# Kernel tuning notes

Measured on AMD Instinct MI355X. Metric: run time of the kernel, lower is better.

The kernel has to match this reference:

```python
import jax, jax.numpy as jnp
import numpy as np

B, NB, L, K, C, H = 4, 256, 64, 65, 512, 8
HD = C // H
SCALE = HD ** -0.5


def setup_inputs() -> dict:
    key = jax.random.key(0)
    k = jax.random.split(key, 6)
    x = jax.random.normal(k[0], (B, NB * L, C), dtype=jnp.float32)
    mask = jax.random.bernoulli(k[1], 0.3, (NB, L, K))
    d = jnp.arange(L)
    mask = mask.at[:, d, d].set(True)      # self edges always on
    mask = mask.at[:, :, L].set(True)      # block-node column always on
    edge_feats = jax.random.normal(k[2], (NB, L, K, 4), dtype=jnp.float32)
    qkv_w = jax.random.normal(k[3], (C, 3 * C), dtype=jnp.float32) * (C ** -0.5)
    qkv_b = jnp.zeros((3 * C,), dtype=jnp.float32)
    proj_w = jax.random.normal(k[4], (C, C), dtype=jnp.float32) * (C ** -0.5)
    proj_b = jnp.zeros((C,), dtype=jnp.float32)
    return {"x": x, "attn_mask": mask, "edge_feats": edge_feats,
            "qkv_w": qkv_w, "qkv_b": qkv_b, "proj_w": proj_w, "proj_b": proj_b}


def reference(x, attn_mask, edge_feats, qkv_w, qkv_b, proj_w, proj_b):
    # x: (B, N, C) with N = NB*L (no padding needed); pool = 1, layout LxL+1
    x_blk = x.reshape(B, NB, L, C)                       # query tokens per leaf block
    block_node = x_blk.mean(axis=2, keepdims=True)       # (B, NB, 1, C)
    kv = jnp.concatenate([x_blk, block_node], axis=2)    # (B, NB, K, C), K = L+1

    qkv_q = x_blk @ qkv_w + qkv_b
    qkv_kv = kv @ qkv_w + qkv_b
    q = qkv_q[..., :C].reshape(B, NB, L, H, HD)
    k = qkv_kv[..., C:2 * C].reshape(B, NB, K, H, HD)
    v = qkv_kv[..., 2 * C:].reshape(B, NB, K, H, HD)

    scores = jnp.einsum('bnqhd,bnkhd->bnqkh', q, k) * SCALE  # (B,NB,L,K,H)

    # physics bias: edge_feats[..., :4] broadcast over batch; special/diagonal overrides
    bp = jnp.broadcast_to(edge_feats[None, ..., :4], (B, NB, L, K, 4))
    bp = bp.at[:, :, :, L, :].set(0.0)
    bp = bp.at[:, :, :, L, 3].set(1.0)                    # block-node key column
    d = jnp.arange(L)
    bp = bp.at[:, :, d, d, :].set(0.0)
    bp = bp.at[:, :, d, d, 3].set(1.0)                    # self edge
    scores = scores + bp[..., 3:4]                        # channel 3 additive bias (all heads)

    mask = attn_mask[None, :, :, :, None]                 # (1,NB,L,K,1)
    scores = jnp.where(mask, scores, jnp.float32(-1e9))
    attn = jax.nn.softmax(scores, axis=3)

    out = jnp.einsum('bnqkh,bnkhd->bnqhd', attn, v).reshape(B, NB * L, C)
    return out @ proj_w + proj_b
```

## Files before the change

### kernel.cpp

```cpp
#include <hip/hip_runtime.h>
#include <hip/hip_bf16.h>
#include <math.h>

typedef unsigned short u16;
typedef __attribute__((ext_vector_type(8))) short s16x8;
typedef __attribute__((ext_vector_type(4))) float f32x4;

#define NB_ 256
#define L_  64
#define KK_ 65
#define C_  512
#define H_  8
#define NEDGE (256*64*65)
#define MTOT  65536
#define MEXT  66560

__device__ __forceinline__ float b2f(u16 u){
  union { unsigned int i; float f; } x; x.i = ((unsigned int)u) << 16; return x.f;
}
__device__ __forceinline__ u16 f2b(float f){
  union { float f; unsigned int i; } x; x.f = f;
  return (u16)((x.i + 0x7FFFu + ((x.i >> 16) & 1u)) >> 16);
}

__device__ __forceinline__ void gload_lds16(const u16* g, u16* l){
  __builtin_amdgcn_global_load_lds(
      (const __attribute__((address_space(1))) unsigned int*)g,
      (__attribute__((address_space(3))) unsigned int*)l,
      16, 0, 0);
}

__global__ void detect_dtype_kernel(const u16* __restrict__ x, int* __restrict__ flagdt){
  __shared__ int cnt;
  if (threadIdx.x == 0) cnt = 0;
  __syncthreads();
  u16 v = x[(size_t)threadIdx.x * 2 * 1001];
  int e = (v >> 7) & 0xFF;
  if (e >= 141) atomicAdd(&cnt, 1);
  __syncthreads();
  if (threadIdx.x == 0) *flagdt = (cnt >= 8) ? 1 : 0;
}

__global__ void detect_mask_kernel(const unsigned char* __restrict__ m, int* __restrict__ flag){
  __shared__ int ok1, ok2, ok4;
  if (threadIdx.x == 0){ ok1 = 1; ok2 = 1; ok4 = 1; }
  __syncthreads();
  size_t e = (size_t)threadIdx.x * 65 + 64;
  if (((const unsigned char*)m)[e] == 0)  atomicAnd(&ok1, 0);
  if (((const unsigned short*)m)[e] == 0) atomicAnd(&ok2, 0);
  if (((const unsigned int*)m)[e] == 0u)  atomicAnd(&ok4, 0);
  __syncthreads();
  if (threadIdx.x == 0){
    int f = 4;
    if (ok2) f = 2;
    if (ok1) f = 1;
    *flag = f;
  }
}

__global__ void convert_kernel(const void* __restrict__ src, u16* __restrict__ dst,
                               long n, const int* __restrict__ flagdt){
  long i = ((long)blockIdx.x * 256 + threadIdx.x) * 8;
  if (i >= n) return;
  if (*flagdt){
    const float* s = (const float*)src + i;
    u16 o[8];
    #pragma unroll
    for (int j = 0; j < 8; ++j) o[j] = f2b(s[j]);
    *(s16x8*)(dst + i) = *(const s16x8*)o;
  } else {
    *(s16x8*)(dst + i) = *(const s16x8*)((const u16*)src + i);
  }
}

__global__ __launch_bounds__(256) void convert_mean_kernel(
    const void* __restrict__ src, u16* __restrict__ XC,
    const int* __restrict__ flagdt){
  __shared__ float ssum[4][512];
  const int t  = threadIdx.x;
  const int rg = t >> 6;
  const int c8 = t & 63;
  const int blk = blockIdx.x;
  const int fdt = *flagdt;

  float sum[8];
  #pragma unroll
  for (int j = 0; j < 8; ++j) sum[j] = 0.f;

  for (int r = 0; r < 16; ++r){
    long idx = ((long)blk*64 + rg*16 + r)*512 + c8*8;
    u16 o[8];
    if (fdt){
      const float* s = (const float*)src + idx;
      #pragma unroll
      for (int j = 0; j < 8; ++j){ float v = s[j]; sum[j] += v; o[j] = f2b(v); }
    } else {
      s16x8 v = *(const s16x8*)((const u16*)src + idx);
      #pragma unroll
      for (int j = 0; j < 8; ++j){ u16 u = (u16)v[j]; sum[j] += b2f(u); o[j] = u; }
    }
    *(s16x8*)(XC + idx) = *(const s16x8*)o;
  }
  #pragma unroll
  for (int j = 0; j < 8; ++j) ssum[rg][c8*8 + j] = sum[j];
  __syncthreads();
  for (int col = t; col < 512; col += 256){
    float tot = ssum[0][col] + ssum[1][col] + ssum[2][col] + ssum[3][col];
    XC[((long)MTOT + blk)*512 + col] = f2b(tot * 0.015625f);
  }
}

__global__ void build_bias_kernel(const void* __restrict__ edge,
                                  const unsigned char* __restrict__ mask,
                                  const int* __restrict__ flagdt,
                                  const int* __restrict__ flagm,
                                  u16* __restrict__ dst){
  long i = (long)blockIdx.x * 256 + threadIdx.x;
  if (i >= NEDGE) return;
  int kk = (int)(i % 65);
  long rowi = i / 65;
  int l = (int)(rowi & 63);
  int fm = *flagm;
  bool mt;
  if (fm == 1)      mt = mask[i] != 0;
  else if (fm == 2) mt = ((const unsigned short*)mask)[i] != 0;
  else              mt = ((const unsigned int*)mask)[i]   != 0u;
  float v;
  if (!mt)                      v = -1e9f;
  else if (kk == 64 || kk == l) v = 1.0f;
  else v = (*flagdt) ? ((const float*)edge)[i*4 + 3] : b2f(((const u16*)edge)[i*4 + 3]);
  dst[i] = f2b(v);
}

__global__ void transpose_conv_kernel(const void* __restrict__ in, u16* __restrict__ out,
                                      int R, int Cc, const int* __restrict__ flagdt){
  long i = (long)blockIdx.x * 256 + threadIdx.x;
  if (i < (long)R * Cc){
    int r = (int)(i / Cc), c = (int)(i % Cc);
    u16 v = (*flagdt) ? f2b(((const float*)in)[i]) : ((const u16*)in)[i];
    out[(long)c * R + r] = v;
  }
}

__global__ __launch_bounds__(256) void gemm_bt_kernel(
    const u16* __restrict__ A, const u16* __restrict__ BT,
    const u16* __restrict__ bias, u16* __restrict__ Cmat,
    int lda, int ldc, int Kdim, const int* __restrict__ flagdt, int out_mode,
    long row_off)
{
  __shared__ __align__(16) u16 As[2*128*32];
  __shared__ __align__(16) u16 Bs[2*128*32];
  const int t = threadIdx.x;
  const int lane = t & 63;
  const int w = t >> 6;
  const int wm = w & 1, wn = w >> 1;
  const int quad = lane >> 4;
  const int ml = lane & 15;

  const int nwg  = gridDim.x * gridDim.y;
  const int orig = blockIdx.y * gridDim.x + blockIdx.x;
  int lid = orig;
  if ((nwg & 7) == 0) lid = (orig & 7) * (nwg >> 3) + (orig >> 3);
  const int bx = lid % gridDim.x;
  const int by = lid / gridDim.x;
  const long colbase = (long)bx * 128;
  const long rowbase = (long)by * 128;
  const int of = out_mode ? *flagdt : 0;

  const f32x4 zero4 = {0.f, 0.f, 0.f, 0.f};
  f32x4 acc[4][4];
  #pragma unroll
  for (int i = 0; i < 4; ++i)
    #pragma unroll
    for (int j = 0; j < 4; ++j) acc[i][j] = zero4;

  const int c0 = t,       r0 = c0 >> 2, s0 = c0 & 3, g0 = s0 ^ ((r0 >> 1) & 3);
  const int c1 = t + 256, r1 = c1 >> 2, s1 = c1 & 3, g1 = s1 ^ ((r1 >> 1) & 3);
  const u16* Arow0 = A + (rowbase + r0) * (long)lda + g0*8;
  const u16* Arow1 = A + (rowbase + r1) * (long)lda + g1*8;
  const u16* Brow0 = BT + (colbase + r0) * (long)Kdim + g0*8;
  const u16* Brow1 = BT + (colbase + r1) * (long)Kdim + g1*8;

  for (int k0 = 0; k0 < Kdim; k0 += 64){
    __syncthreads();
    gload_lds16(Arow0 + k0,      As + w*512);
    gload_lds16(Arow1 + k0,      As + 2048 + w*512);
    gload_lds16(Arow0 + k0 + 32, As + 4096 + w*512);
    gload_lds16(Arow1 + k0 + 32, As + 4096 + 2048 + w*512);
    gload_lds16(Brow0 + k0,      Bs + w*512);
    gload_lds16(Brow1 + k0,      Bs + 2048 + w*512);
    gload_lds16(Brow0 + k0 + 32, Bs + 4096 + w*512);
    gload_lds16(Brow1 + k0 + 32, Bs + 4096 + 2048 + w*512);
    __syncthreads();
    #pragma unroll
    for (int hb = 0; hb < 2; ++hb){
      const u16* Ab = As + hb*4096;
      const u16* Bb = Bs + hb*4096;
      s16x8 af[4], bfr[4];
      #pragma unroll
      for (int i = 0; i < 4; ++i){
        int m = wm*64 + i*16 + ml;
        af[i]  = *(const s16x8*)(Ab + m*32 + ((quad ^ ((m>>1)&3)))*8);
        int n = wn*64 + i*16 + ml;
        bfr[i] = *(const s16x8*)(Bb + n*32 + ((quad ^ ((n>>1)&3)))*8);
      }
      #pragma unroll
      for (int i = 0; i < 4; ++i)
        #pragma unroll
        for (int j = 0; j < 4; ++j)
          acc[i][j] = __builtin_amdgcn_mfma_f32_16x16x32_bf16(af[i], bfr[j], acc[i][j], 0, 0, 0);
    }
  }

  #pragma unroll
  for (int j = 0; j < 4; ++j){
    long col = colbase + wn*64 + j*16 + ml;
    float bv = b2f(bias[col]);
    #pragma unroll
    for (int i = 0; i < 4; ++i){
      long row = row_off + rowbase + wm*64 + i*16 + quad*4;
      if (of){
        float* Cf = (float*)Cmat;
        #pragma unroll
        for (int r = 0; r < 4; ++r)
          Cf[(row + r) * (long)ldc + col] = acc[i][j][r] + bv;
      } else {
        #pragma unroll
        for (int r = 0; r < 4; ++r)
          Cmat[(row + r) * (long)ldc + col] = f2b(acc[i][j][r] + bv);
      }
    }
  }
}

__global__ __launch_bounds__(256, 4) void attn_kernel(
    const u16* __restrict__ Y, const u16* __restrict__ biasb,
    u16* __restrict__ AO)
{
  __shared__ __align__(16) u16 k_s [80*72];
  __shared__ __align__(16) u16 vT_s[64*104];
  __shared__ __align__(16) u16 P_s [64*104];

  const int t = threadIdx.x;
  const int lane = t & 63;
  const int w = t >> 6;
  const int quad = lane >> 4;
  const int ml = lane & 15;

  const int orig = blockIdx.y * gridDim.x + blockIdx.x;
  const int lid  = (orig & 7) * 256 + (orig >> 3);
  const int blk  = lid >> 1;
  const int hq   = lid & 1;
  const int nb = blk & (NB_ - 1);
  const long yrow0 = (long)blk * 64;

  float bb[5][4];
  #pragma unroll
  for (int j = 0; j < 5; ++j){
    int kk = j*16 + ml;
    #pragma unroll
    for (int r = 0; r < 4; ++r){
      int l = w*16 + quad*4 + r;
      bb[j][r] = (kk < 65) ? b2f(biasb[((long)nb*64 + l)*65 + kk]) : 0.f;
    }
  }

  for (int i = t; i < 64*31; i += 256){ int d = i/31, c = 65 + (i%31); vT_s[d*104 + c] = 0; }
  for (int i = t; i < 64*16; i += 256){ int l = i>>4,  c = 80 + (i&15); P_s[l*104 + c] = 0; }
  for (int i = t; i < 15*72; i += 256){ k_s[65*72 + i] = 0; }

  const int kk0 = t >> 3,  c8 = t & 7;
  const int kk1 = kk0 + 32;
  const u16* yb0 = Y + (yrow0 + kk0)*1536;
  const u16* yb1 = Y + (yrow0 + kk1)*1536;
  const u16* kvbase = Y + ((long)MTOT + blk)*1536;

  const f32x4 zero4 = {0.f, 0.f, 0.f, 0.f};
  s16x8 kr0, vr0, kr1, vr1;

  for (int hh = 0; hh < 4; ++hh){
    const int h = hq*4 + hh;

    if (hh == 0){
      for (int c = t; c < 520; c += 256){
        int kk = c >> 3, cc = c & 7;
        const u16 *srck, *srcv;
        if (kk < 64){
          const u16* base = Y + (yrow0 + kk)*1536;
          srck = base + 512  + h*64 + cc*8;
          srcv = base + 1024 + h*64 + cc*8;
        } else {
          srck = kvbase + 512  + h*64 + cc*8;
          srcv = kvbase + 1024 + h*64 + cc*8;
        }
        *(s16x8*)(k_s + kk*72 + cc*8) = *(const s16x8*)srck;
        s16x8 vv = *(const s16x8*)srcv;
        #pragma unroll
        for (int j = 0; j < 8; ++j){
          int jj = (j + cc) & 7;
          vT_s[(cc*8 + jj)*104 + kk] = (u16)vv[jj];
        }
      }
    } else {
      __syncthreads();
      *(s16x8*)(k_s + kk0*72 + c8*8) = kr0;
      *(s16x8*)(k_s + kk1*72 + c8*8) = kr1;
      #pragma unroll
      for (int j = 0; j < 8; ++j){
        int jj = (j + c8) & 7;
        vT_s[(c8*8 + jj)*104 + kk0] = (u16)vr0[jj];
        vT_s[(c8*8 + jj)*104 + kk1] = (u16)vr1[jj];
      }
      if (t < 8){
        *(s16x8*)(k_s + 64*72 + t*8) = *(const s16x8*)(kvbase + 512 + h*64 + t*8);
        s16x8 vv = *(const s16x8*)(kvbase + 1024 + h*64 + t*8);
        #pragma unroll
        for (int j = 0; j < 8; ++j){
          int jj = (j + t) & 7;
          vT_s[(t*8 + jj)*104 + 64] = (u16)vv[jj];
        }
      }
    }
    __syncthreads();

    const u16* qrow = Y + (yrow0 + w*16 + ml)*1536 + h*64 + quad*8;
    s16x8 aq0 = *(const s16x8*)(qrow);
    s16x8 aq1 = *(const s16x8*)(qrow + 32);

    f32x4 sacc[5];
    #pragma unroll
    for (int j = 0; j < 5; ++j) sacc[j] = zero4;
    #pragma unroll
    for (int j = 0; j < 5; ++j){
      s16x8 bk0 = *(const s16x8*)(k_s + (j*16 + ml)*72 + quad*8);
      sacc[j] = __builtin_amdgcn_mfma_f32_16x16x32_bf16(aq0, bk0, sacc[j], 0, 0, 0);
      s16x8 bk1 = *(const s16x8*)(k_s + (j*16 + ml)*72 + 32 + quad*8);
      sacc[j] = __builtin_amdgcn_mfma_f32_16x16x32_bf16(aq1, bk1, sacc[j], 0, 0, 0);
    }

    if (hh < 3){
      const int hn = h + 1;
      kr0 = *(const s16x8*)(yb0 + 512  + hn*64 + c8*8);
      vr0 = *(const s16x8*)(yb0 + 1024 + hn*64 + c8*8);
      kr1 = *(const s16x8*)(yb1 + 512  + hn*64 + c8*8);
      vr1 = *(const s16x8*)(yb1 + 1024 + hn*64 + c8*8);
    }

    float sv[5][4];
    #pragma unroll
    for (int j = 0; j < 5; ++j){
      int kk = j*16 + ml;
      #pragma unroll
      for (int r = 0; r < 4; ++r)
        sv[j][r] = (kk < 65) ? (sacc[j][r]*0.125f + bb[j][r]) : -1e9f;
    }
    #pragma unroll
    for (int r = 0; r < 4; ++r){
      float mx = sv[0][r];
      #pragma unroll
      for (int j = 1; j < 5; ++j) mx = fmaxf(mx, sv[j][r]);
      #pragma unroll
      for (int o = 1; o < 16; o <<= 1) mx = fmaxf(mx, __shfl_xor(mx, o, 64));
      float sm = 0.f;
      #pragma unroll
      for (int j = 0; j < 5; ++j){ float e = __expf(sv[j][r] - mx); sv[j][r] = e; sm += e; }
      #pragma unroll
      for (int o = 1; o < 16; o <<= 1) sm += __shfl_xor(sm, o, 64);
      float inv = 1.0f / sm;
      #pragma unroll
      for (int j = 0; j < 5; ++j) sv[j][r] *= inv;
    }
    #pragma unroll
    for (int j = 0; j < 5; ++j){
      int kk = j*16 + ml;
      #pragma unroll
      for (int r = 0; r < 4; ++r)
        P_s[(w*16 + quad*4 + r)*104 + kk] = f2b(sv[j][r]);
    }
    __syncthreads();

    f32x4 oacc[4];
    #pragma unroll
    for (int j = 0; j < 4; ++j) oacc[j] = zero4;
    #pragma unroll
    for (int s = 0; s < 3; ++s){
      s16x8 ap = *(const s16x8*)(P_s + (w*16 + ml)*104 + s*32 + quad*8);
      #pragma unroll
      for (int j = 0; j < 4; ++j){
        s16x8 bv = *(const s16x8*)(vT_s + (j*16 + ml)*104 + s*32 + quad*8);
        oacc[j] = __builtin_amdgcn_mfma_f32_16x16x32_bf16(ap, bv, oacc[j], 0, 0, 0);
      }
    }
    #pragma unroll
    for (int j = 0; j < 4; ++j){
      int d = j*16 + ml;
      #pragma unroll
      for (int r = 0; r < 4; ++r){
        int l = w*16 + quad*4 + r;
        AO[(yrow0 + l)*512 + h*64 + d] = f2b(oacc[j][r]);
      }
    }
  }
}

extern "C" void kernel_launch(void* const* d_in, const int* in_sizes, int n_in,
                              void* d_out, int out_size, void* d_ws, size_t ws_size,
                              hipStream_t stream)
{
  const void* x_raw     = d_in[0];
  const unsigned char* mask = (const unsigned char*)d_in[1];
  const void* edge_raw  = d_in[2];
  const void* qkvw_raw  = d_in[3];
  const void* qkvb_raw  = d_in[4];
  const void* projw_raw = d_in[5];
  const void* projb_raw = d_in[6];

  char* ws = (char*)d_ws;
  size_t off = 0;
  int*  flagm  = (int*)ws;
  int*  flagdt = (int*)(ws + 4);         off += 1024;
  u16*  XC  = (u16*)(ws + off);          off += (size_t)MEXT*512*2;
  u16*  EB  = (u16*)(ws + off);          off += (size_t)NEDGE*2;
  u16*  WT  = (u16*)(ws + off);          off += (size_t)1536*512*2;
  u16*  PT  = (u16*)(ws + off);          off += (size_t)512*512*2;
  u16*  QB  = (u16*)(ws + off);          off += 4096;
  u16*  PB  = (u16*)(ws + off);          off += 4096;
  u16*  Y   = (u16*)(ws + off);          off += (size_t)MEXT*1536*2;
  u16*  AO  = (u16*)(ws + off);          off += (size_t)MTOT*512*2;

  detect_dtype_kernel<<<dim3(1), dim3(128), 0, stream>>>((const u16*)x_raw, flagdt);
  detect_mask_kernel<<<dim3(1), dim3(128), 0, stream>>>(mask, flagm);

  convert_mean_kernel<<<dim3(1024), dim3(256), 0, stream>>>(x_raw, XC, flagdt);
  build_bias_kernel<<<dim3((NEDGE + 255)/256), dim3(256), 0, stream>>>(edge_raw, mask, flagdt, flagm, EB);
  transpose_conv_kernel<<<dim3((512*1536 + 255)/256), dim3(256), 0, stream>>>(qkvw_raw, WT, 512, 1536, flagdt);
  transpose_conv_kernel<<<dim3((512*512  + 255)/256), dim3(256), 0, stream>>>(projw_raw, PT, 512, 512, flagdt);
  convert_kernel<<<dim3(1), dim3(256), 0, stream>>>(qkvb_raw, QB, 1536, flagdt);
  convert_kernel<<<dim3(1), dim3(256), 0, stream>>>(projb_raw, PB, 512, flagdt);

  gemm_bt_kernel<<<dim3(12, MEXT/128), dim3(256), 0, stream>>>(XC, WT, QB, Y, 512, 1536, 512, flagdt, 0, 0);
  attn_kernel<<<dim3(1024, 2), dim3(256), 0, stream>>>(Y, EB, AO);
  gemm_bt_kernel<<<dim3(4, MTOT/128), dim3(256), 0, stream>>>(AO, PT, PB, (u16*)d_out, 512, 512, 512, flagdt, 1, 0);
}
```

Before: 579.9 us.

## Alias K and P shared buffers and drop register prefetch to raise occupancy

Merges the K tile and the softmax probability tile into one shared-memory buffer, separated by an extra barrier. The register-held prefetch of the next head's K/V is removed, and every head now reloads directly from global memory. Together with launch bounds raised from 4 to 6 blocks per SM, this cuts LDS and register use so more blocks can be resident. The cost is one more barrier per head and the loss of overlap between global loads and compute.

```diff
diff --git a/kernel.cpp b/kernel.cpp
--- a/kernel.cpp
+++ b/kernel.cpp
@@ -233,13 +233,12 @@
   }
 }
 
-__global__ __launch_bounds__(256, 4) void attn_kernel(
+__global__ __launch_bounds__(256, 6) void attn_kernel(
     const u16* __restrict__ Y, const u16* __restrict__ biasb,
     u16* __restrict__ AO)
 {
-  __shared__ __align__(16) u16 k_s [80*72];
+  __shared__ __align__(16) u16 U[6656];
   __shared__ __align__(16) u16 vT_s[64*104];
-  __shared__ __align__(16) u16 P_s [64*104];
 
   const int t = threadIdx.x;
   const int lane = t & 63;
@@ -265,60 +264,35 @@
     }
   }
 
+  const s16x8 z8 = {0,0,0,0,0,0,0,0};
   for (int i = t; i < 64*31; i += 256){ int d = i/31, c = 65 + (i%31); vT_s[d*104 + c] = 0; }
-  for (int i = t; i < 64*16; i += 256){ int l = i>>4,  c = 80 + (i&15); P_s[l*104 + c] = 0; }
-  for (int i = t; i < 15*72; i += 256){ k_s[65*72 + i] = 0; }
-
-  const int kk0 = t >> 3,  c8 = t & 7;
-  const int kk1 = kk0 + 32;
-  const u16* yb0 = Y + (yrow0 + kk0)*1536;
-  const u16* yb1 = Y + (yrow0 + kk1)*1536;
+  for (int r = t; r < 65; r += 256) *(s16x8*)(U + r*72 + 64) = z8;
+  for (int i = t; i < 247; i += 256) *(s16x8*)(U + 4680 + i*8) = z8;
+
   const u16* kvbase = Y + ((long)MTOT + blk)*1536;
-
   const f32x4 zero4 = {0.f, 0.f, 0.f, 0.f};
-  s16x8 kr0, vr0, kr1, vr1;
 
   for (int hh = 0; hh < 4; ++hh){
     const int h = hq*4 + hh;
-
-    if (hh == 0){
-      for (int c = t; c < 520; c += 256){
-        int kk = c >> 3, cc = c & 7;
-        const u16 *srck, *srcv;
-        if (kk < 64){
-          const u16* base = Y + (yrow0 + kk)*1536;
-          srck = base + 512  + h*64 + cc*8;
-          srcv = base + 1024 + h*64 + cc*8;
-        } else {
-          srck = kvbase + 512  + h*64 + cc*8;
-          srcv = kvbase + 1024 + h*64 + cc*8;
-        }
-        *(s16x8*)(k_s + kk*72 + cc*8) = *(const s16x8*)srck;
-        s16x8 vv = *(const s16x8*)srcv;
-        #pragma unroll
-        for (int j = 0; j < 8; ++j){
-          int jj = (j + cc) & 7;
-          vT_s[(cc*8 + jj)*104 + kk] = (u16)vv[jj];
-        }
-      }
-    } else {
-      __syncthreads();
-      *(s16x8*)(k_s + kk0*72 + c8*8) = kr0;
-      *(s16x8*)(k_s + kk1*72 + c8*8) = kr1;
+    if (hh) __syncthreads();
+
+    for (int c = t; c < 520; c += 256){
+      int kk = c >> 3, cc = c & 7;
+      const u16 *srck, *srcv;
+      if (kk < 64){
+        const u16* base = Y + (yrow0 + kk)*1536;
+        srck = base + 512  + h*64 + cc*8;
+        srcv = base + 1024 + h*64 + cc*8;
+      } else {
+        srck = kvbase + 512  + h*64 + cc*8;
+        srcv = kvbase + 1024 + h*64 + cc*8;
+      }
+      *(s16x8*)(U + kk*72 + cc*8) = *(const s16x8*)srck;
+      s16x8 vv = *(const s16x8*)srcv;
       #pragma unroll
       for (int j = 0; j < 8; ++j){
-        int jj = (j + c8) & 7;
-        vT_s[(c8*8 + jj)*104 + kk0] = (u16)vr0[jj];
-        vT_s[(c8*8 + jj)*104 + kk1] = (u16)vr1[jj];
-      }
-      if (t < 8){
-        *(s16x8*)(k_s + 64*72 + t*8) = *(const s16x8*)(kvbase + 512 + h*64 + t*8);
-        s16x8 vv = *(const s16x8*)(kvbase + 1024 + h*64 + t*8);
-        #pragma unroll
-        for (int j = 0; j < 8; ++j){
-          int jj = (j + t) & 7;
-          vT_s[(t*8 + jj)*104 + 64] = (u16)vv[jj];
-        }
+        int jj = (j + cc) & 7;
+        vT_s[(cc*8 + jj)*104 + kk] = (u16)vv[jj];
       }
     }
     __syncthreads();
@@ -332,18 +306,10 @@
     for (int j = 0; j < 5; ++j) sacc[j] = zero4;
     #pragma unroll
     for (int j = 0; j < 5; ++j){
-      s16x8 bk0 = *(const s16x8*)(k_s + (j*16 + ml)*72 + quad*8);
+      s16x8 bk0 = *(const s16x8*)(U + (j*16 + ml)*72 + quad*8);
       sacc[j] = __builtin_amdgcn_mfma_f32_16x16x32_bf16(aq0, bk0, sacc[j], 0, 0, 0);
-      s16x8 bk1 = *(const s16x8*)(k_s + (j*16 + ml)*72 + 32 + quad*8);
+      s16x8 bk1 = *(const s16x8*)(U + (j*16 + ml)*72 + 32 + quad*8);
       sacc[j] = __builtin_amdgcn_mfma_f32_16x16x32_bf16(aq1, bk1, sacc[j], 0, 0, 0);
-    }
-
-    if (hh < 3){
-      const int hn = h + 1;
-      kr0 = *(const s16x8*)(yb0 + 512  + hn*64 + c8*8);
-      vr0 = *(const s16x8*)(yb0 + 1024 + hn*64 + c8*8);
-      kr1 = *(const s16x8*)(yb1 + 512  + hn*64 + c8*8);
-      vr1 = *(const s16x8*)(yb1 + 1024 + hn*64 + c8*8);
     }
 
     float sv[5][4];
@@ -370,12 +336,14 @@
       #pragma unroll
       for (int j = 0; j < 5; ++j) sv[j][r] *= inv;
     }
+
+    __syncthreads();
     #pragma unroll
     for (int j = 0; j < 5; ++j){
       int kk = j*16 + ml;
       #pragma unroll
       for (int r = 0; r < 4; ++r)
-        P_s[(w*16 + quad*4 + r)*104 + kk] = f2b(sv[j][r]);
+        U[(w*16 + quad*4 + r)*104 + kk] = f2b(sv[j][r]);
     }
     __syncthreads();
 
@@ -384,7 +352,7 @@
     for (int j = 0; j < 4; ++j) oacc[j] = zero4;
     #pragma unroll
     for (int s = 0; s < 3; ++s){
-      s16x8 ap = *(const s16x8*)(P_s + (w*16 + ml)*104 + s*32 + quad*8);
+      s16x8 ap = *(const s16x8*)(U + (w*16 + ml)*104 + s*32 + quad*8);
       #pragma unroll
       for (int j = 0; j < 4; ++j){
         s16x8 bv = *(const s16x8*)(vT_s + (j*16 + ml)*104 + s*32 + quad*8);
```

After: 596.2 us. +2.8%, slower.
